# Optimization experiments

Measured on AMD Instinct MI355X. Metric: run time of the kernel, lower is better.

## Reference

```python
import jax, jax.numpy as jnp
import numpy as np

B, S, D = 2, 2048, 1024
H, KVH, HD = 16, 4, 64
ROPE_THETA = 10000.0


def rotate_half(x):
    h = x.shape[-1] // 2
    return jnp.concatenate([-x[..., h:], x[..., :h]], axis=-1)


def setup_inputs() -> dict:
    key = jax.random.key(0)
    k = jax.random.split(key, 6)
    x = jax.random.normal(k[0], (B, S, D), dtype=jnp.float32)
    # real RoPE tables: [S, HD//2]
    inv_freq = 1.0 / (ROPE_THETA ** (jnp.arange(0, HD, 2, dtype=jnp.float32) / HD))
    t = jnp.arange(S, dtype=jnp.float32)
    freqs = jnp.outer(t, inv_freq)  # [S, HD/2]
    cos = jnp.cos(freqs)
    sin = jnp.sin(freqs)
    # causal additive mask [1,1,S,S]
    neg = jnp.float32(-1e9)
    mask = jnp.where(jnp.tril(jnp.ones((S, S), dtype=bool)), 0.0, neg)[None, None]
    scale = 0.02
    wq = jax.random.normal(k[1], (D, H * HD), dtype=jnp.float32) * scale
    wk = jax.random.normal(k[2], (D, KVH * HD), dtype=jnp.float32) * scale
    wv = jax.random.normal(k[3], (D, KVH * HD), dtype=jnp.float32) * scale
    wo = jax.random.normal(k[4], (H * HD, D), dtype=jnp.float32) * scale
    return {"x": x, "cos": cos, "sin": sin, "mask": mask,
            "wq": wq, "wk": wk, "wv": wv, "wo": wo}


def reference(x, cos, sin, mask, wq, wk, wv, wo):
    b, s, d = x.shape
    hd = 2 * cos.shape[-1]
    h = wq.shape[1] // hd
    kvh = wk.shape[1] // hd
    n_rep = h // kvh

    q = (x @ wq).reshape(b, s, h, hd)
    k = (x @ wk).reshape(b, s, kvh, hd)
    v = (x @ wv).reshape(b, s, kvh, hd)

    # RoPE: cos/sin [S, hd/2] -> [1, s, 1, hd] via self-concat (rotate_half style)
    c = jnp.concatenate([cos[:s], cos[:s]], axis=-1)[None, :, None, :]
    sn = jnp.concatenate([sin[:s], sin[:s]], axis=-1)[None, :, None, :]
    q = q * c + rotate_half(q) * sn
    k = k * c + rotate_half(k) * sn

    new_k, new_v = k, v  # kv cache (pre-repeat)

    # GQA: repeat each kv head n_rep times contiguously (== expand+reshape)
    if n_rep > 1:
        k = jnp.repeat(k, n_rep, axis=2)
        v = jnp.repeat(v, n_rep, axis=2)

    scores = jnp.einsum('bqhd,bkhd->bhqk', q, k) / jnp.sqrt(jnp.float32(hd))
    scores = scores + mask
    attn = jax.nn.softmax(scores.astype(jnp.float32), axis=-1).astype(q.dtype)
    out = jnp.einsum('bhqk,bkhd->bqhd', attn, v).reshape(b, s, h * hd)
    out = out @ wo
    return (out, new_k, new_v)
```

## Files before the change

### kernel.cpp

```cpp
#include <hip/hip_runtime.h>
#include <hip/hip_bf16.h>

constexpr int B_ = 2, S_ = 2048, D_ = 1024, H_ = 16, KVH_ = 4, HD_ = 64;

typedef __attribute__((ext_vector_type(8))) short short8;
typedef __attribute__((ext_vector_type(4))) float f32x4;
typedef __attribute__((ext_vector_type(16))) float f32x16;

__device__ inline short f2b(float x) {
  unsigned u = __float_as_uint(x);
  return (short)((u + 0x7fffu + ((u >> 16) & 1u)) >> 16);
}
__device__ inline unsigned pkbf2(float lo, float hi) {
  __hip_bfloat162 h = __float22bfloat162_rn(float2{lo, hi});
  return *(unsigned*)&h;
}

__device__ inline void async16(void* lds, const void* g) {
  __builtin_amdgcn_global_load_lds(
      (const __attribute__((address_space(1))) unsigned int*)g,
      (__attribute__((address_space(3))) unsigned int*)lds, 16, 0, 0);
}

__global__ __launch_bounds__(256) void prep_kernel(
    const float* __restrict__ x, short* __restrict__ xb,
    const float* __restrict__ wq, const float* __restrict__ wk,
    const float* __restrict__ wv, const float* __restrict__ wo,
    short* __restrict__ wt, short* __restrict__ wot) {
  __shared__ short ts[64][66];
  const int tid = threadIdx.x;
  if (blockIdx.x < 4096) {
    const int idx = (blockIdx.x * 256 + tid) * 4;
    float4 v = *(const float4*)(x + idx);
    short4 o;
    o.x = f2b(v.x); o.y = f2b(v.y); o.z = f2b(v.z); o.w = f2b(v.w);
    *(short4*)(xb + idx) = o;
    return;
  }
  const int bid = blockIdx.x - 4096;
  const int z = bid >> 8, bi = (bid >> 4) & 15, bj = bid & 15;
  const float* W;
  short* dst;
  int N;
  if (z == 0)      { W = wq; dst = wt;                       N = 1024; }
  else if (z == 1) { W = wo; dst = wot;                      N = 1024; }
  else if (z == 2) { W = wk; dst = wt + (size_t)1024 * 1024; N = 256; }
  else             { W = wv; dst = wt + (size_t)1280 * 1024; N = 256; }
  if (bj * 64 >= N) return;
#pragma unroll
  for (int i = 0; i < 16; ++i) {
    int idx = tid + i * 256;
    int r = idx >> 6, c = idx & 63;
    ts[r][c] = f2b(W[(size_t)(bi * 64 + r) * N + bj * 64 + c]);
  }
  __syncthreads();
#pragma unroll
  for (int i = 0; i < 16; ++i) {
    int idx = tid + i * 256;
    int cc = idx >> 6, rr = idx & 63;
    dst[(size_t)(bj * 64 + cc) * 1024 + bi * 64 + rr] = ts[rr][cc];
  }
}

struct GemmLdsDb {
  short As[2][128][32];
  short Bs[2][128][32];
};

__device__ inline void gemm_core_db(GemmLdsDb& lds, const short* __restrict__ A,
                                    const short* __restrict__ Bt, int K,
                                    int row0, int col0, int tid,
                                    f32x4 (&acc)[4][4]) {
  const int w = tid >> 6, lane = tid & 63;
  const int grp = lane >> 4, li = lane & 15;
  const int wr = w & 1, wc = w >> 1;
  const int lr = lane >> 2, ls = (lane & 3) * 8;
#pragma unroll
  for (int mt = 0; mt < 4; ++mt)
#pragma unroll
    for (int nt = 0; nt < 4; ++nt) acc[mt][nt] = (f32x4){0.f, 0.f, 0.f, 0.f};

  auto issue = [&](int bi, int k0) {
#pragma unroll
    for (int i = 0; i < 2; ++i) {
      const int r = i * 64 + w * 16;
      async16(&lds.As[bi][r][0], A + (size_t)(row0 + r + lr) * K + k0 + ls);
      async16(&lds.Bs[bi][r][0], Bt + (size_t)(col0 + r + lr) * K + k0 + ls);
    }
  };

  issue(0, 0);
  const int nk = K >> 5;
  for (int kk = 0; kk < nk; ++kk) {
    const int cur = kk & 1;
    __syncthreads();
    if (kk + 1 < nk) issue(cur ^ 1, (kk + 1) << 5);

    short8 af[4], bf[4];
#pragma unroll
    for (int mt = 0; mt < 4; ++mt)
      af[mt] = *(const short8*)&lds.As[cur][wr * 64 + mt * 16 + li][grp * 8];
#pragma unroll
    for (int nt = 0; nt < 4; ++nt)
      bf[nt] = *(const short8*)&lds.Bs[cur][wc * 64 + nt * 16 + li][grp * 8];
#pragma unroll
    for (int mt = 0; mt < 4; ++mt)
#pragma unroll
      for (int nt = 0; nt < 4; ++nt)
        acc[mt][nt] = __builtin_amdgcn_mfma_f32_16x16x32_bf16(
            af[mt], bf[nt], acc[mt][nt], 0, 0, 0);
  }
}

#define QSCALE 0.1803368801111f

__global__ __launch_bounds__(256) void gemm_qkv(
    const short* __restrict__ A, const short* __restrict__ Bt,
    const float* __restrict__ cs, const float* __restrict__ sn,
    short* __restrict__ qb, float* __restrict__ koutp, short* __restrict__ kb,
    float* __restrict__ voutp, short* __restrict__ vbT) {
  __shared__ GemmLdsDb lds;
  const int tid = threadIdx.x;
  const int w = tid >> 6, lane = tid & 63;
  const int grp = lane >> 4, li = lane & 15;
  const int wr = w & 1, wc = w >> 1;
  const int row0 = blockIdx.y * 128, col0 = blockIdx.x * 128;
  f32x4 acc[4][4];
  gemm_core_db(lds, A, Bt, D_, row0, col0, tid, acc);

  if (col0 < 1024) {
#pragma unroll
    for (int mt = 0; mt < 4; ++mt)
#pragma unroll
      for (int r = 0; r < 4; ++r) {
        const int row = row0 + wr * 64 + mt * 16 + grp * 4 + r;
        const int spos = row & (S_ - 1);
#pragma unroll
        for (int nt = 0; nt < 2; ++nt) {
          const int col = col0 + wc * 64 + nt * 16 + li;
          const int d = col & 63;
          const float c = cs[spos * 32 + d];
          const float s = sn[spos * 32 + d];
          const float x0 = acc[mt][nt][r], x1 = acc[mt][nt + 2][r];
          qb[(size_t)row * 1024 + col] = f2b((x0 * c - x1 * s) * QSCALE);
          qb[(size_t)row * 1024 + col + 32] = f2b((x1 * c + x0 * s) * QSCALE);
        }
      }
  } else if (col0 < 1280) {
#pragma unroll
    for (int mt = 0; mt < 4; ++mt)
#pragma unroll
      for (int r = 0; r < 4; ++r) {
        const int row = row0 + wr * 64 + mt * 16 + grp * 4 + r;
        const int bq = row >> 11, spos = row & (S_ - 1);
        const int sb = spos >> 5, k32 = spos & 31;
#pragma unroll
        for (int nt = 0; nt < 2; ++nt) {
          const int kcol = col0 + wc * 64 + nt * 16 + li - 1024;
          const int khk = kcol >> 6, d = kcol & 63;
          const float c = cs[spos * 32 + d];
          const float s = sn[spos * 32 + d];
          const float x0 = acc[mt][nt][r], x1 = acc[mt][nt + 2][r];
          const float k0v = x0 * c - x1 * s;
          const float k1v = x1 * c + x0 * s;
          koutp[(size_t)row * 256 + kcol] = k0v;
          koutp[(size_t)row * 256 + kcol + 32] = k1v;
          short* kbase =
              kb + (((size_t)(bq * 4 + khk) * 64 + sb) * 2048) + k32 * 8;
          const int d2 = d + 32;
          kbase[((d >> 4) * 2 + ((d >> 3) & 1)) * 256 + (d & 7)] = f2b(k0v);
          kbase[((d2 >> 4) * 2 + ((d2 >> 3) & 1)) * 256 + (d2 & 7)] = f2b(k1v);
        }
      }
  } else {
#pragma unroll
    for (int mt = 0; mt < 4; ++mt)
#pragma unroll
      for (int nt = 0; nt < 4; ++nt) {
        const int vcol = col0 + wc * 64 + nt * 16 + li - 1280;
        const int row_base = row0 + wr * 64 + mt * 16 + grp * 4;
        short4 pk;
        float vv[4];
#pragma unroll
        for (int r = 0; r < 4; ++r) vv[r] = acc[mt][nt][r];
        pk.x = f2b(vv[0]); pk.y = f2b(vv[1]);
        pk.z = f2b(vv[2]); pk.w = f2b(vv[3]);
#pragma unroll
        for (int r = 0; r < 4; ++r)
          voutp[(size_t)(row_base + r) * 256 + vcol] = vv[r];
        const int bq = row_base >> 11, s0 = row_base & (S_ - 1);
        const int t = s0 >> 6, k64 = s0 & 63;
        const int kc = k64 >> 4, kg8 = (k64 >> 3) & 1, k8 = k64 & 7;
        const int khv = vcol >> 6, d = vcol & 63;
        short* vb = vbT + (((size_t)(bq * 4 + khv) * 32 + t) * 4096) +
                    (d >> 5) * 2048 + kc * 512 + kg8 * 256 + (d & 31) * 8 + k8;
        *(short4*)vb = pk;
      }
  }
}

__global__ __launch_bounds__(128) void fattn_kernel(
    const short* __restrict__ qb, const short* __restrict__ kb,
    const short* __restrict__ vbT, short* __restrict__ o) {
  __shared__ float scr[64 * 33 + 32];

  const int tid = threadIdx.x;
  const int par = tid >> 6, lane = tid & 63;
  const int n32 = lane & 31, kg = lane >> 5;

  const int qt = 63 - (blockIdx.x >> 5);
  const int bh = blockIdx.x & 31;
  const int b = bh >> 4, h = bh & 15, kh = h >> 2;
  const int qq = qt >> 1, st = qt & 1;
  const int nt = qq + 1;

  const short* qp =
      qb + ((size_t)(b * S_ + qt * 32 + n32)) * 1024 + h * 64 + kg * 8;
  short8 qa[4];
#pragma unroll
  for (int ks = 0; ks < 4; ++ks) qa[ks] = *(const short8*)(qp + ks * 16);

  const short* kF = kb + ((size_t)(b * 4 + kh) << 17) + lane * 8;
  const short* vF = vbT + ((size_t)(b * 4 + kh) << 17) + lane * 8;

  f32x16 zero16;
#pragma unroll
  for (int i = 0; i < 16; ++i) zero16[i] = 0.f;
  f32x16 Oa0 = zero16, Oa1 = zero16;
  float lreg = 0.f;

  auto loadK = [&](int t, short8 (&kr)[8]) {
    const short* kt = kF + (size_t)t * 4096;
#pragma unroll
    for (int s = 0; s < 2; ++s)
#pragma unroll
      for (int ks = 0; ks < 4; ++ks)
        kr[s * 4 + ks] = *(const short8*)(kt + s * 2048 + ks * 512);
  };

  auto body = [&](int t, const short8 (&kr)[8], short8 (&knx)[8]) {
    const bool diag = (t == qq);
    const short* vt = vF + (size_t)t * 4096;
    short8 vr[8];
#pragma unroll
    for (int kc = 0; kc < 4; ++kc) {
      vr[kc] = *(const short8*)(vt + kc * 512);
      vr[kc + 4] = *(const short8*)(vt + 2048 + kc * 512);
    }
    if (t + 2 < nt) loadK(t + 2, knx);

    unsigned pk[4][4];
#pragma unroll
    for (int s = 0; s < 2; ++s) {
      if (s == 1 && diag && st == 0) continue;
      f32x16 sv = __builtin_amdgcn_mfma_f32_32x32x16_bf16(kr[s * 4 + 0], qa[0],
                                                          zero16, 0, 0, 0);
      sv = __builtin_amdgcn_mfma_f32_32x32x16_bf16(kr[s * 4 + 1], qa[1], sv, 0,
                                                   0, 0);
      sv = __builtin_amdgcn_mfma_f32_32x32x16_bf16(kr[s * 4 + 2], qa[2], sv, 0,
                                                   0, 0);
      sv = __builtin_amdgcn_mfma_f32_32x32x16_bf16(kr[s * 4 + 3], qa[3], sv, 0,
                                                   0, 0);
      const bool dm = diag && (s == st);
      float e[16];
#pragma unroll
      for (int rr = 0; rr < 16; ++rr) {
        float v = __builtin_amdgcn_exp2f(sv[rr]);
        if (dm) {
          const int key32 = (rr & 3) + 8 * (rr >> 2) + 4 * kg;
          if (key32 > n32) v = 0.f;
        }
        e[rr] = v;
      }
      pk[2 * s][0] = pkbf2(e[0], e[1]);
      pk[2 * s][1] = pkbf2(e[2], e[3]);
      pk[2 * s][2] = pkbf2(e[4], e[5]);
      pk[2 * s][3] = pkbf2(e[6], e[7]);
      pk[2 * s + 1][0] = pkbf2(e[8], e[9]);
      pk[2 * s + 1][1] = pkbf2(e[10], e[11]);
      pk[2 * s + 1][2] = pkbf2(e[12], e[13]);
      pk[2 * s + 1][3] = pkbf2(e[14], e[15]);
      lreg += (((e[0] + e[1]) + (e[2] + e[3])) +
               ((e[4] + e[5]) + (e[6] + e[7]))) +
              (((e[8] + e[9]) + (e[10] + e[11])) +
               ((e[12] + e[13]) + (e[14] + e[15])));
    }

    auto pv = [&](int kc) {
      auto r02 =
          __builtin_amdgcn_permlane32_swap(pk[kc][0], pk[kc][2], false, false);
      auto r13 =
          __builtin_amdgcn_permlane32_swap(pk[kc][1], pk[kc][3], false, false);
      union { unsigned u[4]; short8 s8; } f;
      f.u[0] = r02[0]; f.u[1] = r13[0]; f.u[2] = r02[1]; f.u[3] = r13[1];
      Oa0 = __builtin_amdgcn_mfma_f32_32x32x16_bf16(vr[kc], f.s8, Oa0, 0, 0, 0);
      Oa1 = __builtin_amdgcn_mfma_f32_32x32x16_bf16(vr[kc + 4], f.s8, Oa1, 0,
                                                    0, 0);
    };
    if (diag && st == 0) {
      pv(0); pv(1);
    } else {
      pv(0); pv(1); pv(2); pv(3);
    }
  };

  {
    short8 kA[8], kB[8];
    int t = par;
    if (t < nt) {
      loadK(t, kA);
      for (;;) {
        body(t, kA, kB);
        t += 2;
        if (t >= nt) break;
        body(t, kB, kA);
        t += 2;
        if (t >= nt) break;
      }
    }
  }

  lreg += __shfl_xor(lreg, 32);

  float* lb = scr + 64 * 33;
  if (par == 1) {
#pragma unroll
    for (int rr = 0; rr < 16; ++rr) {
      const int d0 = (rr & 3) + 8 * (rr >> 2) + 4 * kg;
      scr[d0 * 33 + n32] = Oa0[rr];
      scr[(d0 + 32) * 33 + n32] = Oa1[rr];
    }
    if (kg == 0) lb[n32] = lreg;
  }
  __syncthreads();
  if (par == 0) {
    const float inv = __builtin_amdgcn_rcpf(lreg + lb[n32]);
#pragma unroll
    for (int rr = 0; rr < 16; ++rr) {
      const int d0 = (rr & 3) + 8 * (rr >> 2) + 4 * kg;
      scr[d0 * 33 + n32] = (Oa0[rr] + scr[d0 * 33 + n32]) * inv;
      scr[(d0 + 32) * 33 + n32] = (Oa1[rr] + scr[(d0 + 32) * 33 + n32]) * inv;
    }
  }
  __syncthreads();
  {
    const int q = tid >> 2, seg = (tid & 3) * 16;
    const size_t gb = ((size_t)(b * S_ + qt * 32 + q)) * 1024 + h * 64 + seg;
    short8 t0, t1;
#pragma unroll
    for (int k2 = 0; k2 < 8; ++k2) {
      t0[k2] = f2b(scr[(seg + k2) * 33 + q]);
      t1[k2] = f2b(scr[(seg + 8 + k2) * 33 + q]);
    }
    *(short8*)(o + gb) = t0;
    *(short8*)(o + gb + 8) = t1;
  }
}

__global__ __launch_bounds__(256) void gemm_bt_f32(
    const short* __restrict__ A, const short* __restrict__ Bt,
    float* __restrict__ C, int N, int K) {
  __shared__ GemmLdsDb lds;
  const int tid = threadIdx.x;
  const int w = tid >> 6, lane = tid & 63;
  const int grp = lane >> 4, li = lane & 15;
  const int wr = w & 1, wc = w >> 1;
  const int row0 = blockIdx.y * 128, col0 = blockIdx.x * 128;
  f32x4 acc[4][4];
  gemm_core_db(lds, A, Bt, K, row0, col0, tid, acc);
#pragma unroll
  for (int mt = 0; mt < 4; ++mt)
#pragma unroll
    for (int nt = 0; nt < 4; ++nt)
#pragma unroll
      for (int r = 0; r < 4; ++r)
        C[(size_t)(row0 + wr * 64 + mt * 16 + grp * 4 + r) * N + col0 +
          wc * 64 + nt * 16 + li] = acc[mt][nt][r];
}

extern "C" void kernel_launch(void* const* d_in, const int* in_sizes, int n_in,
                              void* d_out, int out_size, void* d_ws,
                              size_t ws_size, hipStream_t stream) {
  const float* x  = (const float*)d_in[0];
  const float* cs = (const float*)d_in[1];
  const float* sn = (const float*)d_in[2];
  const float* wq = (const float*)d_in[4];
  const float* wk = (const float*)d_in[5];
  const float* wv = (const float*)d_in[6];
  const float* wo = (const float*)d_in[7];

  float* outp  = (float*)d_out;
  float* koutp = outp + (size_t)B_ * S_ * H_ * HD_;
  float* voutp = koutp + (size_t)B_ * S_ * KVH_ * HD_;

  char* p = (char*)d_ws;
  short* xb   = (short*)p; p += (size_t)B_ * S_ * D_ * 2;
  short* qb   = (short*)p; p += (size_t)B_ * S_ * H_ * HD_ * 2;
  short* kb   = (short*)p; p += (size_t)B_ * S_ * KVH_ * HD_ * 2;
  short* vbT  = (short*)p; p += (size_t)B_ * S_ * KVH_ * HD_ * 2;
  short* abuf = (short*)p; p += (size_t)B_ * S_ * H_ * HD_ * 2;
  short* wt   = (short*)p; p += (size_t)1536 * D_ * 2;
  short* wot  = (short*)p; p += (size_t)D_ * H_ * HD_ * 2;

  const int M = B_ * S_;

  prep_kernel<<<4096 + 1024, 256, 0, stream>>>(x, xb, wq, wk, wv, wo, wt,
                                               wot);

  gemm_qkv<<<dim3(1536 / 128, M / 128), 256, 0, stream>>>(
      xb, wt, cs, sn, qb, koutp, kb, voutp, vbT);

  fattn_kernel<<<64 * 32, 128, 0, stream>>>(qb, kb, vbT, abuf);

  gemm_bt_f32<<<dim3(1024 / 128, M / 128), 256, 0, stream>>>(abuf, wot, outp,
                                                             1024, 1024);
}
```

Baseline: 171.7 us.

## Shrink GEMM tiles to 64x128 and prefetch V with K in attention

Both projection GEMMs move from 128x128 to 64x128 output tiles, with each wave owning a 16-row strip across all 128 columns. This doubles the grid so more CUs have work on M=4096. The attention kernel now prefetches the V tile for the next iteration together with K, and raises wave priority around the MFMA sections with s_setprio. The cost is lower data reuse per tile and more register pressure from the double-buffered V.

Result: no change. 172.0 us (+0.2%).

```diff
diff --git a/kernel.cpp b/kernel.cpp
--- a/kernel.cpp
+++ b/kernel.cpp
@@ -62,30 +62,28 @@
   }
 }
 
-struct GemmLdsDb {
-  short As[2][128][32];
+struct GemmLds64 {
+  short As[2][64][32];
   short Bs[2][128][32];
 };
 
-__device__ inline void gemm_core_db(GemmLdsDb& lds, const short* __restrict__ A,
-                                    const short* __restrict__ Bt, int K,
-                                    int row0, int col0, int tid,
-                                    f32x4 (&acc)[4][4]) {
+__device__ inline void gemm_core64(GemmLds64& lds, const short* __restrict__ A,
+                                   const short* __restrict__ Bt, int K,
+                                   int row0, int col0, int tid,
+                                   f32x4 (&acc)[8]) {
   const int w = tid >> 6, lane = tid & 63;
   const int grp = lane >> 4, li = lane & 15;
-  const int wr = w & 1, wc = w >> 1;
-  const int lr = lane >> 2, ls = (lane & 3) * 8;
-#pragma unroll
-  for (int mt = 0; mt < 4; ++mt)
-#pragma unroll
-    for (int nt = 0; nt < 4; ++nt) acc[mt][nt] = (f32x4){0.f, 0.f, 0.f, 0.f};
+#pragma unroll
+  for (int nt = 0; nt < 8; ++nt) acc[nt] = (f32x4){0.f, 0.f, 0.f, 0.f};
 
   auto issue = [&](int bi, int k0) {
+    async16((short*)&lds.As[bi][0][0] + tid * 8,
+            A + (size_t)(row0 + (tid >> 2)) * K + k0 + (tid & 3) * 8);
 #pragma unroll
     for (int i = 0; i < 2; ++i) {
-      const int r = i * 64 + w * 16;
-      async16(&lds.As[bi][r][0], A + (size_t)(row0 + r + lr) * K + k0 + ls);
-      async16(&lds.Bs[bi][r][0], Bt + (size_t)(col0 + r + lr) * K + k0 + ls);
+      const int idx = i * 256 + tid;
+      async16((short*)&lds.Bs[bi][0][0] + idx * 8,
+              Bt + (size_t)(col0 + (idx >> 2)) * K + k0 + (idx & 3) * 8);
     }
   };
 
@@ -96,19 +94,15 @@
     __syncthreads();
     if (kk + 1 < nk) issue(cur ^ 1, (kk + 1) << 5);
 
-    short8 af[4], bf[4];
-#pragma unroll
-    for (int mt = 0; mt < 4; ++mt)
-      af[mt] = *(const short8*)&lds.As[cur][wr * 64 + mt * 16 + li][grp * 8];
-#pragma unroll
-    for (int nt = 0; nt < 4; ++nt)
-      bf[nt] = *(const short8*)&lds.Bs[cur][wc * 64 + nt * 16 + li][grp * 8];
-#pragma unroll
-    for (int mt = 0; mt < 4; ++mt)
-#pragma unroll
-      for (int nt = 0; nt < 4; ++nt)
-        acc[mt][nt] = __builtin_amdgcn_mfma_f32_16x16x32_bf16(
-            af[mt], bf[nt], acc[mt][nt], 0, 0, 0);
+    const short8 af = *(const short8*)&lds.As[cur][w * 16 + li][grp * 8];
+    short8 bf[8];
+#pragma unroll
+    for (int nt = 0; nt < 8; ++nt)
+      bf[nt] = *(const short8*)&lds.Bs[cur][nt * 16 + li][grp * 8];
+#pragma unroll
+    for (int nt = 0; nt < 8; ++nt)
+      acc[nt] = __builtin_amdgcn_mfma_f32_16x16x32_bf16(af, bf[nt], acc[nt],
+                                                        0, 0, 0);
   }
 }
 
@@ -119,48 +113,49 @@
     const float* __restrict__ cs, const float* __restrict__ sn,
     short* __restrict__ qb, float* __restrict__ koutp, short* __restrict__ kb,
     float* __restrict__ voutp, short* __restrict__ vbT) {
-  __shared__ GemmLdsDb lds;
+  __shared__ GemmLds64 lds;
   const int tid = threadIdx.x;
   const int w = tid >> 6, lane = tid & 63;
   const int grp = lane >> 4, li = lane & 15;
-  const int wr = w & 1, wc = w >> 1;
-  const int row0 = blockIdx.y * 128, col0 = blockIdx.x * 128;
-  f32x4 acc[4][4];
-  gemm_core_db(lds, A, Bt, D_, row0, col0, tid, acc);
+  const int row0 = blockIdx.y * 64, col0 = blockIdx.x * 128;
+  f32x4 acc[8];
+  gemm_core64(lds, A, Bt, D_, row0, col0, tid, acc);
 
   if (col0 < 1024) {
 #pragma unroll
-    for (int mt = 0; mt < 4; ++mt)
-#pragma unroll
-      for (int r = 0; r < 4; ++r) {
-        const int row = row0 + wr * 64 + mt * 16 + grp * 4 + r;
-        const int spos = row & (S_ - 1);
-#pragma unroll
-        for (int nt = 0; nt < 2; ++nt) {
-          const int col = col0 + wc * 64 + nt * 16 + li;
-          const int d = col & 63;
+    for (int h2 = 0; h2 < 2; ++h2)
+#pragma unroll
+      for (int p = 0; p < 2; ++p) {
+        const int nt = h2 * 4 + p;
+#pragma unroll
+        for (int r = 0; r < 4; ++r) {
+          const int row = row0 + w * 16 + grp * 4 + r;
+          const int spos = row & (S_ - 1);
+          const int col = col0 + nt * 16 + li;
+          const int d = p * 16 + li;
           const float c = cs[spos * 32 + d];
           const float s = sn[spos * 32 + d];
-          const float x0 = acc[mt][nt][r], x1 = acc[mt][nt + 2][r];
+          const float x0 = acc[nt][r], x1 = acc[nt + 2][r];
           qb[(size_t)row * 1024 + col] = f2b((x0 * c - x1 * s) * QSCALE);
           qb[(size_t)row * 1024 + col + 32] = f2b((x1 * c + x0 * s) * QSCALE);
         }
       }
   } else if (col0 < 1280) {
 #pragma unroll
-    for (int mt = 0; mt < 4; ++mt)
-#pragma unroll
-      for (int r = 0; r < 4; ++r) {
-        const int row = row0 + wr * 64 + mt * 16 + grp * 4 + r;
-        const int bq = row >> 11, spos = row & (S_ - 1);
-        const int sb = spos >> 5, k32 = spos & 31;
-#pragma unroll
-        for (int nt = 0; nt < 2; ++nt) {
-          const int kcol = col0 + wc * 64 + nt * 16 + li - 1024;
+    for (int h2 = 0; h2 < 2; ++h2)
+#pragma unroll
+      for (int p = 0; p < 2; ++p) {
+        const int nt = h2 * 4 + p;
+#pragma unroll
+        for (int r = 0; r < 4; ++r) {
+          const int row = row0 + w * 16 + grp * 4 + r;
+          const int bq = row >> 11, spos = row & (S_ - 1);
+          const int sb = spos >> 5, k32 = spos & 31;
+          const int kcol = col0 + nt * 16 + li - 1024;
           const int khk = kcol >> 6, d = kcol & 63;
           const float c = cs[spos * 32 + d];
           const float s = sn[spos * 32 + d];
-          const float x0 = acc[mt][nt][r], x1 = acc[mt][nt + 2][r];
+          const float x0 = acc[nt][r], x1 = acc[nt + 2][r];
           const float k0v = x0 * c - x1 * s;
           const float k1v = x1 * c + x0 * s;
           koutp[(size_t)row * 256 + kcol] = k0v;
@@ -174,28 +169,26 @@
       }
   } else {
 #pragma unroll
-    for (int mt = 0; mt < 4; ++mt)
-#pragma unroll
-      for (int nt = 0; nt < 4; ++nt) {
-        const int vcol = col0 + wc * 64 + nt * 16 + li - 1280;
-        const int row_base = row0 + wr * 64 + mt * 16 + grp * 4;
-        short4 pk;
-        float vv[4];
-#pragma unroll
-        for (int r = 0; r < 4; ++r) vv[r] = acc[mt][nt][r];
-        pk.x = f2b(vv[0]); pk.y = f2b(vv[1]);
-        pk.z = f2b(vv[2]); pk.w = f2b(vv[3]);
-#pragma unroll
-        for (int r = 0; r < 4; ++r)
-          voutp[(size_t)(row_base + r) * 256 + vcol] = vv[r];
-        const int bq = row_base >> 11, s0 = row_base & (S_ - 1);
-        const int t = s0 >> 6, k64 = s0 & 63;
-        const int kc = k64 >> 4, kg8 = (k64 >> 3) & 1, k8 = k64 & 7;
-        const int khv = vcol >> 6, d = vcol & 63;
-        short* vb = vbT + (((size_t)(bq * 4 + khv) * 32 + t) * 4096) +
-                    (d >> 5) * 2048 + kc * 512 + kg8 * 256 + (d & 31) * 8 + k8;
-        *(short4*)vb = pk;
-      }
+    for (int nt = 0; nt < 8; ++nt) {
+      const int vcol = col0 + nt * 16 + li - 1280;
+      const int row_base = row0 + w * 16 + grp * 4;
+      short4 pk;
+      float vv[4];
+#pragma unroll
+      for (int r = 0; r < 4; ++r) vv[r] = acc[nt][r];
+      pk.x = f2b(vv[0]); pk.y = f2b(vv[1]);
+      pk.z = f2b(vv[2]); pk.w = f2b(vv[3]);
+#pragma unroll
+      for (int r = 0; r < 4; ++r)
+        voutp[(size_t)(row_base + r) * 256 + vcol] = vv[r];
+      const int bq = row_base >> 11, s0 = row_base & (S_ - 1);
+      const int t = s0 >> 6, k64 = s0 & 63;
+      const int kc = k64 >> 4, kg8 = (k64 >> 3) & 1, k8 = k64 & 7;
+      const int khv = vcol >> 6, d = vcol & 63;
+      short* vb = vbT + (((size_t)(bq * 4 + khv) * 32 + t) * 4096) +
+                  (d >> 5) * 2048 + kc * 512 + kg8 * 256 + (d & 31) * 8 + k8;
+      *(short4*)vb = pk;
+    }
   }
 }
 
@@ -237,22 +230,22 @@
       for (int ks = 0; ks < 4; ++ks)
         kr[s * 4 + ks] = *(const short8*)(kt + s * 2048 + ks * 512);
   };
-
-  auto body = [&](int t, const short8 (&kr)[8], short8 (&knx)[8]) {
-    const bool diag = (t == qq);
+  auto loadV = [&](int t, short8 (&vr)[8]) {
     const short* vt = vF + (size_t)t * 4096;
-    short8 vr[8];
 #pragma unroll
     for (int kc = 0; kc < 4; ++kc) {
       vr[kc] = *(const short8*)(vt + kc * 512);
       vr[kc + 4] = *(const short8*)(vt + 2048 + kc * 512);
     }
-    if (t + 2 < nt) loadK(t + 2, knx);
-
+  };
+
+  auto body = [&](int t, const short8 (&kr)[8], const short8 (&vr)[8]) {
+    const bool diag = (t == qq);
     unsigned pk[4][4];
 #pragma unroll
     for (int s = 0; s < 2; ++s) {
       if (s == 1 && diag && st == 0) continue;
+      __builtin_amdgcn_s_setprio(1);
       f32x16 sv = __builtin_amdgcn_mfma_f32_32x32x16_bf16(kr[s * 4 + 0], qa[0],
                                                           zero16, 0, 0, 0);
       sv = __builtin_amdgcn_mfma_f32_32x32x16_bf16(kr[s * 4 + 1], qa[1], sv, 0,
@@ -261,6 +254,7 @@
                                                    0, 0);
       sv = __builtin_amdgcn_mfma_f32_32x32x16_bf16(kr[s * 4 + 3], qa[3], sv, 0,
                                                    0, 0);
+      __builtin_amdgcn_s_setprio(0);
       const bool dm = diag && (s == st);
       float e[16];
 #pragma unroll
@@ -297,23 +291,28 @@
       Oa1 = __builtin_amdgcn_mfma_f32_32x32x16_bf16(vr[kc + 4], f.s8, Oa1, 0,
                                                     0, 0);
     };
+    __builtin_amdgcn_s_setprio(1);
     if (diag && st == 0) {
       pv(0); pv(1);
     } else {
       pv(0); pv(1); pv(2); pv(3);
     }
+    __builtin_amdgcn_s_setprio(0);
   };
 
   {
-    short8 kA[8], kB[8];
+    short8 kA[8], kB[8], vA[8], vB[8];
     int t = par;
     if (t < nt) {
       loadK(t, kA);
+      loadV(t, vA);
       for (;;) {
-        body(t, kA, kB);
+        if (t + 2 < nt) { loadV(t + 2, vB); loadK(t + 2, kB); }
+        body(t, kA, vA);
         t += 2;
         if (t >= nt) break;
-        body(t, kB, kA);
+        if (t + 2 < nt) { loadV(t + 2, vA); loadK(t + 2, kA); }
+        body(t, kB, vB);
         t += 2;
         if (t >= nt) break;
       }
@@ -360,22 +359,19 @@
 __global__ __launch_bounds__(256) void gemm_bt_f32(
     const short* __restrict__ A, const short* __restrict__ Bt,
     float* __restrict__ C, int N, int K) {
-  __shared__ GemmLdsDb lds;
+  __shared__ GemmLds64 lds;
   const int tid = threadIdx.x;
   const int w = tid >> 6, lane = tid & 63;
   const int grp = lane >> 4, li = lane & 15;
-  const int wr = w & 1, wc = w >> 1;
-  const int row0 = blockIdx.y * 128, col0 = blockIdx.x * 128;
-  f32x4 acc[4][4];
-  gemm_core_db(lds, A, Bt, K, row0, col0, tid, acc);
-#pragma unroll
-  for (int mt = 0; mt < 4; ++mt)
-#pragma unroll
-    for (int nt = 0; nt < 4; ++nt)
-#pragma unroll
-      for (int r = 0; r < 4; ++r)
-        C[(size_t)(row0 + wr * 64 + mt * 16 + grp * 4 + r) * N + col0 +
-          wc * 64 + nt * 16 + li] = acc[mt][nt][r];
+  const int row0 = blockIdx.y * 64, col0 = blockIdx.x * 128;
+  f32x4 acc[8];
+  gemm_core64(lds, A, Bt, K, row0, col0, tid, acc);
+#pragma unroll
+  for (int nt = 0; nt < 8; ++nt)
+#pragma unroll
+    for (int r = 0; r < 4; ++r)
+      C[(size_t)(row0 + w * 16 + grp * 4 + r) * N + col0 + nt * 16 + li] =
+          acc[nt][r];
 }
 
 extern "C" void kernel_launch(void* const* d_in, const int* in_sizes, int n_in,
@@ -407,11 +403,11 @@
   prep_kernel<<<4096 + 1024, 256, 0, stream>>>(x, xb, wq, wk, wv, wo, wt,
                                                wot);
 
-  gemm_qkv<<<dim3(1536 / 128, M / 128), 256, 0, stream>>>(
+  gemm_qkv<<<dim3(1536 / 128, M / 64), 256, 0, stream>>>(
       xb, wt, cs, sn, qb, koutp, kb, voutp, vbT);
 
   fattn_kernel<<<64 * 32, 128, 0, stream>>>(qb, kb, vbT, abuf);
 
-  gemm_bt_f32<<<dim3(1024 / 128, M / 128), 256, 0, stream>>>(abuf, wot, outp,
-                                                             1024, 1024);
-}
+  gemm_bt_f32<<<dim3(1024 / 128, M / 64), 256, 0, stream>>>(abuf, wot, outp,
+                                                            1024, 1024);
+}
```

## Pair causal query tiles per block and split keys across four waves

Applied to the files above, without the earlier changes.

The attention kernel now runs 256 threads per block and handles two query tiles per block, a light one (pr) and a heavy one (63-pr), so every block gets a similar amount of causal work. Key tiles are strided across four waves instead of two, and the partial results are summed through shared memory with a sequential per-wave reduction. The manual double-buffered K prefetch is dropped, so each iteration loads K and V directly, which may expose more memory latency. The extra barriers and reduction steps add overhead, and the grid is halved.

Result: slower. 190.5 us (+11.0%).

```diff
diff --git a/kernel.cpp b/kernel.cpp
--- a/kernel.cpp
+++ b/kernel.cpp
@@ -199,26 +199,18 @@
   }
 }
 
-__global__ __launch_bounds__(128) void fattn_kernel(
+__global__ __launch_bounds__(256) void fattn_kernel(
     const short* __restrict__ qb, const short* __restrict__ kb,
     const short* __restrict__ vbT, short* __restrict__ o) {
   __shared__ float scr[64 * 33 + 32];
 
   const int tid = threadIdx.x;
-  const int par = tid >> 6, lane = tid & 63;
+  const int w = tid >> 6, lane = tid & 63;
   const int n32 = lane & 31, kg = lane >> 5;
 
-  const int qt = 63 - (blockIdx.x >> 5);
+  const int pr = blockIdx.x >> 5;
   const int bh = blockIdx.x & 31;
   const int b = bh >> 4, h = bh & 15, kh = h >> 2;
-  const int qq = qt >> 1, st = qt & 1;
-  const int nt = qq + 1;
-
-  const short* qp =
-      qb + ((size_t)(b * S_ + qt * 32 + n32)) * 1024 + h * 64 + kg * 8;
-  short8 qa[4];
-#pragma unroll
-  for (int ks = 0; ks < 4; ++ks) qa[ks] = *(const short8*)(qp + ks * 16);
 
   const short* kF = kb + ((size_t)(b * 4 + kh) << 17) + lane * 8;
   const short* vF = vbT + ((size_t)(b * 4 + kh) << 17) + lane * 8;
@@ -226,134 +218,147 @@
   f32x16 zero16;
 #pragma unroll
   for (int i = 0; i < 16; ++i) zero16[i] = 0.f;
-  f32x16 Oa0 = zero16, Oa1 = zero16;
-  float lreg = 0.f;
-
-  auto loadK = [&](int t, short8 (&kr)[8]) {
-    const short* kt = kF + (size_t)t * 4096;
-#pragma unroll
-    for (int s = 0; s < 2; ++s)
-#pragma unroll
-      for (int ks = 0; ks < 4; ++ks)
-        kr[s * 4 + ks] = *(const short8*)(kt + s * 2048 + ks * 512);
-  };
-
-  auto body = [&](int t, const short8 (&kr)[8], short8 (&knx)[8]) {
-    const bool diag = (t == qq);
-    const short* vt = vF + (size_t)t * 4096;
-    short8 vr[8];
-#pragma unroll
-    for (int kc = 0; kc < 4; ++kc) {
-      vr[kc] = *(const short8*)(vt + kc * 512);
-      vr[kc + 4] = *(const short8*)(vt + 2048 + kc * 512);
-    }
-    if (t + 2 < nt) loadK(t + 2, knx);
-
-    unsigned pk[4][4];
-#pragma unroll
-    for (int s = 0; s < 2; ++s) {
-      if (s == 1 && diag && st == 0) continue;
-      f32x16 sv = __builtin_amdgcn_mfma_f32_32x32x16_bf16(kr[s * 4 + 0], qa[0],
-                                                          zero16, 0, 0, 0);
-      sv = __builtin_amdgcn_mfma_f32_32x32x16_bf16(kr[s * 4 + 1], qa[1], sv, 0,
-                                                   0, 0);
-      sv = __builtin_amdgcn_mfma_f32_32x32x16_bf16(kr[s * 4 + 2], qa[2], sv, 0,
-                                                   0, 0);
-      sv = __builtin_amdgcn_mfma_f32_32x32x16_bf16(kr[s * 4 + 3], qa[3], sv, 0,
-                                                   0, 0);
-      const bool dm = diag && (s == st);
-      float e[16];
+
+  for (int pass = 0; pass < 2; ++pass) {
+    const int qt = pass ? (63 - pr) : pr;
+    const int qq = qt >> 1, st = qt & 1;
+    const int nt = qq + 1;
+
+    const short* qp =
+        qb + ((size_t)(b * S_ + qt * 32 + n32)) * 1024 + h * 64 + kg * 8;
+    short8 qa[4];
+#pragma unroll
+    for (int ks = 0; ks < 4; ++ks) qa[ks] = *(const short8*)(qp + ks * 16);
+
+    f32x16 Oa0 = zero16, Oa1 = zero16;
+    float lreg = 0.f;
+
+    for (int t = w; t < nt; t += 4) {
+      const bool diag = (t == qq);
+      const short* kt = kF + (size_t)t * 4096;
+      const short* vt = vF + (size_t)t * 4096;
+      short8 kr[8], vr[8];
+#pragma unroll
+      for (int s = 0; s < 2; ++s)
+#pragma unroll
+        for (int ks = 0; ks < 4; ++ks)
+          kr[s * 4 + ks] = *(const short8*)(kt + s * 2048 + ks * 512);
+#pragma unroll
+      for (int kc = 0; kc < 4; ++kc) {
+        vr[kc] = *(const short8*)(vt + kc * 512);
+        vr[kc + 4] = *(const short8*)(vt + 2048 + kc * 512);
+      }
+
+      unsigned pk[4][4];
+#pragma unroll
+      for (int s = 0; s < 2; ++s) {
+        if (s == 1 && diag && st == 0) continue;
+        f32x16 sv = __builtin_amdgcn_mfma_f32_32x32x16_bf16(
+            kr[s * 4 + 0], qa[0], zero16, 0, 0, 0);
+        sv = __builtin_amdgcn_mfma_f32_32x32x16_bf16(kr[s * 4 + 1], qa[1], sv,
+                                                     0, 0, 0);
+        sv = __builtin_amdgcn_mfma_f32_32x32x16_bf16(kr[s * 4 + 2], qa[2], sv,
+                                                     0, 0, 0);
+        sv = __builtin_amdgcn_mfma_f32_32x32x16_bf16(kr[s * 4 + 3], qa[3], sv,
+                                                     0, 0, 0);
+        const bool dm = diag && (s == st);
+        float e[16];
+#pragma unroll
+        for (int rr = 0; rr < 16; ++rr) {
+          float v = __builtin_amdgcn_exp2f(sv[rr]);
+          if (dm) {
+            const int key32 = (rr & 3) + 8 * (rr >> 2) + 4 * kg;
+            if (key32 > n32) v = 0.f;
+          }
+          e[rr] = v;
+        }
+        pk[2 * s][0] = pkbf2(e[0], e[1]);
+        pk[2 * s][1] = pkbf2(e[2], e[3]);
+        pk[2 * s][2] = pkbf2(e[4], e[5]);
+        pk[2 * s][3] = pkbf2(e[6], e[7]);
+        pk[2 * s + 1][0] = pkbf2(e[8], e[9]);
+        pk[2 * s + 1][1] = pkbf2(e[10], e[11]);
+        pk[2 * s + 1][2] = pkbf2(e[12], e[13]);
+        pk[2 * s + 1][3] = pkbf2(e[14], e[15]);
+        lreg += (((e[0] + e[1]) + (e[2] + e[3])) +
+                 ((e[4] + e[5]) + (e[6] + e[7]))) +
+                (((e[8] + e[9]) + (e[10] + e[11])) +
+                 ((e[12] + e[13]) + (e[14] + e[15])));
+      }
+
+      auto pv = [&](int kc) {
+        auto r02 = __builtin_amdgcn_permlane32_swap(pk[kc][0], pk[kc][2],
+                                                    false, false);
+        auto r13 = __builtin_amdgcn_permlane32_swap(pk[kc][1], pk[kc][3],
+                                                    false, false);
+        union { unsigned u[4]; short8 s8; } f;
+        f.u[0] = r02[0]; f.u[1] = r13[0]; f.u[2] = r02[1]; f.u[3] = r13[1];
+        Oa0 = __builtin_amdgcn_mfma_f32_32x32x16_bf16(vr[kc], f.s8, Oa0, 0, 0,
+                                                      0);
+        Oa1 = __builtin_amdgcn_mfma_f32_32x32x16_bf16(vr[kc + 4], f.s8, Oa1, 0,
+                                                      0, 0);
+      };
+      if (diag && st == 0) {
+        pv(0); pv(1);
+      } else {
+        pv(0); pv(1); pv(2); pv(3);
+      }
+    }
+
+    lreg += __shfl_xor(lreg, 32);
+
+    float* lb = scr + 64 * 33;
+    if (w == 3) {
 #pragma unroll
       for (int rr = 0; rr < 16; ++rr) {
-        float v = __builtin_amdgcn_exp2f(sv[rr]);
-        if (dm) {
-          const int key32 = (rr & 3) + 8 * (rr >> 2) + 4 * kg;
-          if (key32 > n32) v = 0.f;
-        }
-        e[rr] = v;
-      }
-      pk[2 * s][0] = pkbf2(e[0], e[1]);
-      pk[2 * s][1] = pkbf2(e[2], e[3]);
-      pk[2 * s][2] = pkbf2(e[4], e[5]);
-      pk[2 * s][3] = pkbf2(e[6], e[7]);
-      pk[2 * s + 1][0] = pkbf2(e[8], e[9]);
-      pk[2 * s + 1][1] = pkbf2(e[10], e[11]);
-      pk[2 * s + 1][2] = pkbf2(e[12], e[13]);
-      pk[2 * s + 1][3] = pkbf2(e[14], e[15]);
-      lreg += (((e[0] + e[1]) + (e[2] + e[3])) +
-               ((e[4] + e[5]) + (e[6] + e[7]))) +
-              (((e[8] + e[9]) + (e[10] + e[11])) +
-               ((e[12] + e[13]) + (e[14] + e[15])));
-    }
-
-    auto pv = [&](int kc) {
-      auto r02 =
-          __builtin_amdgcn_permlane32_swap(pk[kc][0], pk[kc][2], false, false);
-      auto r13 =
-          __builtin_amdgcn_permlane32_swap(pk[kc][1], pk[kc][3], false, false);
-      union { unsigned u[4]; short8 s8; } f;
-      f.u[0] = r02[0]; f.u[1] = r13[0]; f.u[2] = r02[1]; f.u[3] = r13[1];
-      Oa0 = __builtin_amdgcn_mfma_f32_32x32x16_bf16(vr[kc], f.s8, Oa0, 0, 0, 0);
-      Oa1 = __builtin_amdgcn_mfma_f32_32x32x16_bf16(vr[kc + 4], f.s8, Oa1, 0,
-                                                    0, 0);
-    };
-    if (diag && st == 0) {
-      pv(0); pv(1);
-    } else {
-      pv(0); pv(1); pv(2); pv(3);
-    }
-  };
-
-  {
-    short8 kA[8], kB[8];
-    int t = par;
-    if (t < nt) {
-      loadK(t, kA);
-      for (;;) {
-        body(t, kA, kB);
-        t += 2;
-        if (t >= nt) break;
-        body(t, kB, kA);
-        t += 2;
-        if (t >= nt) break;
-      }
-    }
-  }
-
-  lreg += __shfl_xor(lreg, 32);
-
-  float* lb = scr + 64 * 33;
-  if (par == 1) {
-#pragma unroll
-    for (int rr = 0; rr < 16; ++rr) {
-      const int d0 = (rr & 3) + 8 * (rr >> 2) + 4 * kg;
-      scr[d0 * 33 + n32] = Oa0[rr];
-      scr[(d0 + 32) * 33 + n32] = Oa1[rr];
-    }
-    if (kg == 0) lb[n32] = lreg;
-  }
-  __syncthreads();
-  if (par == 0) {
-    const float inv = __builtin_amdgcn_rcpf(lreg + lb[n32]);
-#pragma unroll
-    for (int rr = 0; rr < 16; ++rr) {
-      const int d0 = (rr & 3) + 8 * (rr >> 2) + 4 * kg;
-      scr[d0 * 33 + n32] = (Oa0[rr] + scr[d0 * 33 + n32]) * inv;
-      scr[(d0 + 32) * 33 + n32] = (Oa1[rr] + scr[(d0 + 32) * 33 + n32]) * inv;
-    }
-  }
-  __syncthreads();
-  {
-    const int q = tid >> 2, seg = (tid & 3) * 16;
-    const size_t gb = ((size_t)(b * S_ + qt * 32 + q)) * 1024 + h * 64 + seg;
-    short8 t0, t1;
-#pragma unroll
-    for (int k2 = 0; k2 < 8; ++k2) {
-      t0[k2] = f2b(scr[(seg + k2) * 33 + q]);
-      t1[k2] = f2b(scr[(seg + 8 + k2) * 33 + q]);
-    }
-    *(short8*)(o + gb) = t0;
-    *(short8*)(o + gb + 8) = t1;
+        const int d0 = (rr & 3) + 8 * (rr >> 2) + 4 * kg;
+        scr[d0 * 33 + n32] = Oa0[rr];
+        scr[(d0 + 32) * 33 + n32] = Oa1[rr];
+      }
+      if (kg == 0) lb[n32] = lreg;
+    }
+    __syncthreads();
+    if (w == 2) {
+#pragma unroll
+      for (int rr = 0; rr < 16; ++rr) {
+        const int d0 = (rr & 3) + 8 * (rr >> 2) + 4 * kg;
+        scr[d0 * 33 + n32] += Oa0[rr];
+        scr[(d0 + 32) * 33 + n32] += Oa1[rr];
+      }
+      if (kg == 0) lb[n32] += lreg;
+    }
+    __syncthreads();
+    if (w == 1) {
+#pragma unroll
+      for (int rr = 0; rr < 16; ++rr) {
+        const int d0 = (rr & 3) + 8 * (rr >> 2) + 4 * kg;
+        scr[d0 * 33 + n32] += Oa0[rr];
+        scr[(d0 + 32) * 33 + n32] += Oa1[rr];
+      }
+      if (kg == 0) lb[n32] += lreg;
+    }
+    __syncthreads();
+    if (w == 0) {
+      const float inv = __builtin_amdgcn_rcpf(lreg + lb[n32]);
+#pragma unroll
+      for (int rr = 0; rr < 16; ++rr) {
+        const int d0 = (rr & 3) + 8 * (rr >> 2) + 4 * kg;
+        scr[d0 * 33 + n32] = (Oa0[rr] + scr[d0 * 33 + n32]) * inv;
+        scr[(d0 + 32) * 33 + n32] =
+            (Oa1[rr] + scr[(d0 + 32) * 33 + n32]) * inv;
+      }
+    }
+    __syncthreads();
+    {
+      const int q = tid >> 3, seg8 = (tid & 7) * 8;
+      const size_t gb =
+          ((size_t)(b * S_ + qt * 32 + q)) * 1024 + h * 64 + seg8;
+      short8 t0;
+#pragma unroll
+      for (int k2 = 0; k2 < 8; ++k2) t0[k2] = f2b(scr[(seg8 + k2) * 33 + q]);
+      *(short8*)(o + gb) = t0;
+    }
+    __syncthreads();
   }
 }
 
@@ -410,7 +415,7 @@
   gemm_qkv<<<dim3(1536 / 128, M / 128), 256, 0, stream>>>(
       xb, wt, cs, sn, qb, koutp, kb, voutp, vbT);
 
-  fattn_kernel<<<64 * 32, 128, 0, stream>>>(qb, kb, vbT, abuf);
+  fattn_kernel<<<32 * 32, 256, 0, stream>>>(qb, kb, vbT, abuf);
 
   gemm_bt_f32<<<dim3(1024 / 128, M / 128), 256, 0, stream>>>(abuf, wot, outp,
                                                              1024, 1024);
```
